# Optimization experiments

Measured on AMD Instinct MI355X. Metric: run time of the kernel, lower is better.

Reference implementation:

```python
import jax, jax.numpy as jnp
import numpy as np

B, DIM, OC, H, W, HEADS = 4, 128, 128, 128, 128, 8
L = H * W
_BN_INV = 1.0 / (1.0 + 1e-5) ** 0.5  # eval-mode BN: running_mean=0, running_var=1


def conv2d(x, w, b=None, groups=1, pad=0):
    y = jax.lax.conv_general_dilated(
        x, w, (1, 1), [(pad, pad), (pad, pad)],
        dimension_numbers=('NCHW', 'OIHW', 'NCHW'),
        feature_group_count=groups)
    if b is not None:
        y = y + b[None, :, None, None]
    return y


def bn(x, g, b):
    return x * (g * _BN_INV)[None, :, None, None] + b[None, :, None, None]


def ln(x, g, b, eps=1e-5):
    m = jnp.mean(x, -1, keepdims=True)
    v = jnp.mean((x - m) ** 2, -1, keepdims=True)
    return (x - m) * jax.lax.rsqrt(v + eps) * g + b


def rope_tables(h, w, c, base=10000.0):
    k_max = c // 4
    theta = 1.0 / base ** (np.arange(k_max, dtype=np.float32) / k_max)
    gi, gj = np.meshgrid(np.arange(h, dtype=np.float32),
                         np.arange(w, dtype=np.float32), indexing='ij')
    ang = np.concatenate([gi[..., None] * theta, gj[..., None] * theta], -1)  # (h,w,c//2)
    return jnp.asarray(np.cos(ang)), jnp.asarray(np.sin(ang))


def apply_rope(x, cs, sn):  # x: (b,h,w,c); consecutive pairs = (re, im)
    xr, xi = x[..., 0::2], x[..., 1::2]
    return jnp.stack([cs * xr - sn * xi, sn * xr + cs * xi], -1).reshape(x.shape)


def linear_attn(x, qk_w, qk_b, lepe_w, lepe_b, h, w):
    b, n, c = x.shape
    hd = c // HEADS
    qk = x @ qk_w.T + qk_b
    q = jax.nn.elu(qk[..., :c]) + 1.0
    k = jax.nn.elu(qk[..., c:]) + 1.0
    cs, sn = rope_tables(h, w, c)

    def heads(t):  # (b,n,c) -> (b,HEADS,n,hd)
        return t.reshape(b, n, HEADS, hd).transpose(0, 2, 1, 3)

    q_r = heads(apply_rope(q.reshape(b, h, w, c), cs, sn).reshape(b, n, c))
    k_r = heads(apply_rope(k.reshape(b, h, w, c), cs, sn).reshape(b, n, c))
    qh, kh, vh = heads(q), heads(k), heads(x)
    k_mean = jnp.mean(kh, axis=2, keepdims=True)                      # (b,Hd,1,hd)
    z = 1.0 / (jnp.einsum('bhnd,bhmd->bhnm', qh, k_mean) + 1e-6)      # (b,Hd,n,1)
    s = n ** -0.5
    kv = jnp.einsum('bhnd,bhne->bhde', k_r * s, vh * s)               # (b,Hd,hd,hd)
    out = jnp.einsum('bhnd,bhde->bhne', q_r, kv) * z
    out = out.transpose(0, 2, 1, 3).reshape(b, n, c)
    v_img = x.reshape(b, h, w, c).transpose(0, 3, 1, 2)
    lepe = conv2d(v_img, lepe_w, lepe_b, groups=c, pad=1)
    return out + lepe.transpose(0, 2, 3, 1).reshape(b, n, c)


def fmt_block(xb, fw1, fb1, f_g, f_be, fw2, fb2, n_g, n_be):
    t = jnp.fft.fft2(xb)                                              # (B,C,H,W) complex
    wgt = jax.nn.relu(bn(conv2d(t.real, fw1, fb1), f_g, f_be))
    wgt = jax.nn.sigmoid(conv2d(wgt, fw2, fb2))
    f = jnp.abs(jnp.fft.ifft2(wgt * t))
    f = jax.nn.relu(bn(f, n_g, n_be))
    return f.reshape(f.shape[0], f.shape[1], -1).transpose(0, 2, 1)   # (B,L,C)


def _forward(x, c1_w, c1_b, c1_g, c1_be, cpe1_w, cpe1_b,
             fw1, fb1, f_g, f_be, fw2, fb2, nbn_g, nbn_be,
             ln1_g, ln1_b, d3w1, d3b1, d3w2, d5w1, d5b1, d5w2,
             ap_w, ap_b, ip2_w, ip2_b, dwc2_w, dwc2_b,
             qk_w, qk_b, lepe_w, lepe_b, op_w, op_b,
             cpe2_w, cpe2_b, ln2_g, ln2_b,
             ffn_w1, ffn_b1, ffn_w2, ffn_b2, po_w,
             red_w, red_b, red_g, red_be):
    Bb, C, Hh, Ww = x.shape
    Ll = Hh * Ww
    to_img = lambda t: t.reshape(Bb, Hh, Ww, C).transpose(0, 3, 1, 2)   # (B,L,C)->(B,C,H,W)
    to_seq = lambda t: t.transpose(0, 2, 3, 1).reshape(Bb, Ll, -1)       # (B,C,H,W)->(B,L,C)

    x_0 = jax.nn.relu(bn(conv2d(x, c1_w, c1_b), c1_g, c1_be))           # (B,OC,H,W)
    xt = to_seq(x + conv2d(x, cpe1_w, cpe1_b, groups=C, pad=1))
    shortcut = xt
    fmt1 = fmt_block(to_img(xt), fw1, fb1, f_g, f_be, fw2, fb2, nbn_g, nbn_be)

    x_s = ln(xt, ln1_g, ln1_b)
    xs_img = to_img(x_s)
    x_s3 = conv2d(conv2d(xs_img, d3w1, d3b1), d3w2, None, groups=C // 2, pad=1)
    x_s5 = conv2d(conv2d(xs_img, d5w1, d5b1), d5w2, None, groups=C // 2, pad=2)
    act_res = jax.nn.silu(to_seq(conv2d(xs_img, ap_w, ap_b)))

    def branch(t):  # (B,C/2,H,W) -> (B,L,C/2)
        t = conv2d(t, ip2_w, ip2_b)
        t = jax.nn.silu(conv2d(t, dwc2_w, dwc2_b, groups=C // 2, pad=1))
        return to_seq(t)

    a3 = linear_attn(branch(x_s3), qk_w, qk_b, lepe_w, lepe_b, Hh, Ww)
    a5 = linear_attn(branch(x_s5), qk_w, qk_b, lepe_w, lepe_b, Hh, Ww)
    xs = jnp.concatenate([a3, a5], -1)
    xs = to_seq(conv2d(to_img(xs * act_res), op_w, op_b))

    xt = shortcut + xs + fmt1
    xt = xt + to_seq(conv2d(to_img(xt), cpe2_w, cpe2_b, groups=C, pad=1))
    fmt2 = fmt_block(to_img(xt), fw1, fb1, f_g, f_be, fw2, fb2, nbn_g, nbn_be)
    h2 = ln(xt, ln2_g, ln2_b)
    ffn = jax.nn.gelu(h2 @ ffn_w1.T + ffn_b1, approximate=False) @ ffn_w2.T + ffn_b2
    xt = xt + ffn + fmt2

    xo = conv2d(to_img(xt), po_w)                                        # (B,OC,H,W)
    cat = jnp.concatenate([x_0, xo], 1)
    return jax.nn.relu(bn(conv2d(cat, red_w, red_b), red_g, red_be)) + x_0


def setup_inputs():
    key = jax.random.key(0)
    it = iter(jax.random.split(key, 64))

    def w(shape, s=0.05):
        return jax.random.normal(next(it), shape, jnp.float32) * s

    d, oc = DIM, OC
    ones = lambda n: jnp.ones((n,), jnp.float32)
    zeros = lambda n: jnp.zeros((n,), jnp.float32)
    return {
        'x': jax.random.normal(next(it), (B, d, H, W), jnp.float32),
        'c1_w': w((oc, d, 1, 1)), 'c1_b': w((oc,), 0.01), 'c1_g': ones(oc), 'c1_be': zeros(oc),
        'cpe1_w': w((d, 1, 3, 3)), 'cpe1_b': w((d,), 0.01),
        'fw1': w((d // 16, d, 1, 1)), 'fb1': w((d // 16,), 0.01),
        'f_g': ones(d // 16), 'f_be': zeros(d // 16),
        'fw2': w((d, d // 16, 1, 1)), 'fb2': w((d,), 0.01),
        'nbn_g': ones(d), 'nbn_be': zeros(d),
        'ln1_g': ones(d), 'ln1_b': zeros(d),
        'd3w1': w((d, d, 1, 1)), 'd3b1': w((d,), 0.01), 'd3w2': w((d // 2, 2, 3, 3)),
        'd5w1': w((d, d, 1, 1)), 'd5b1': w((d,), 0.01), 'd5w2': w((d // 2, 2, 5, 5)),
        'ap_w': w((d, d, 1, 1)), 'ap_b': w((d,), 0.01),
        'ip2_w': w((d // 2, d // 2, 1, 1)), 'ip2_b': w((d // 2,), 0.01),
        'dwc2_w': w((d // 2, 1, 3, 3)), 'dwc2_b': w((d // 2,), 0.01),
        'qk_w': w((d, d // 2)), 'qk_b': w((d,), 0.01),
        'lepe_w': w((d // 2, 1, 3, 3)), 'lepe_b': w((d // 2,), 0.01),
        'op_w': w((d, d, 1, 1)), 'op_b': w((d,), 0.01),
        'cpe2_w': w((d, 1, 3, 3)), 'cpe2_b': w((d,), 0.01),
        'ln2_g': ones(d), 'ln2_b': zeros(d),
        'ffn_w1': w((4, d)), 'ffn_b1': w((4,), 0.01),
        'ffn_w2': w((d, 4)), 'ffn_b2': w((d,), 0.01),
        'po_w': w((oc, d, 1, 1)),
        'red_w': w((oc, 2 * oc, 1, 1)), 'red_b': w((oc,), 0.01),
        'red_g': ones(oc), 'red_be': zeros(oc),
    }


def reference(x, c1_w, c1_b, c1_g, c1_be, cpe1_w, cpe1_b,
              fw1, fb1, f_g, f_be, fw2, fb2, nbn_g, nbn_be,
              ln1_g, ln1_b, d3w1, d3b1, d3w2, d5w1, d5b1, d5w2,
              ap_w, ap_b, ip2_w, ip2_b, dwc2_w, dwc2_b,
              qk_w, qk_b, lepe_w, lepe_b, op_w, op_b,
              cpe2_w, cpe2_b, ln2_g, ln2_b,
              ffn_w1, ffn_b1, ffn_w2, ffn_b2, po_w,
              red_w, red_b, red_g, red_be):
    return _forward(x, c1_w, c1_b, c1_g, c1_be, cpe1_w, cpe1_b,
                    fw1, fb1, f_g, f_be, fw2, fb2, nbn_g, nbn_be,
                    ln1_g, ln1_b, d3w1, d3b1, d3w2, d5w1, d5b1, d5w2,
                    ap_w, ap_b, ip2_w, ip2_b, dwc2_w, dwc2_b,
                    qk_w, qk_b, lepe_w, lepe_b, op_w, op_b,
                    cpe2_w, cpe2_b, ln2_g, ln2_b,
                    ffn_w1, ffn_b1, ffn_w2, ffn_b2, po_w,
                    red_w, red_b, red_g, red_be)
```

## Files before the change

### kernel.cpp

```cpp
#include <hip/hip_runtime.h>
#include <math.h>

typedef unsigned short bf16_t;
typedef __attribute__((ext_vector_type(8))) short short8;
typedef __attribute__((ext_vector_type(4))) float f32x4;

#define B_ 4
#define C_ 128
#define H_ 128
#define W_ 128
#define L_ (H_*W_)
#define NS  ((size_t)B_*L_*C_)
#define NH  ((size_t)B_*L_*64)
#define NSP ((size_t)L_*C_)
#define PI_F 3.14159265358979323846f
#define BN_INV 0.9999950000374997f
#define THETA_SC 0.8304820237218406f
#define TOTW 157148
#define W16SHIFT 107548
#define WOFF_PO 107612
#define WOFF_RED 123996

#define W2_ 66
#define L2_ (128*W2_)
// ... 272 lines not shown
  __syncthreads();
  for (int i = tid; i < 4224; i += 256) {
    int h = i / 33, wl = i - h*33;
    rp[(size_t)h*W2_ + wl] = Lre[h][wl];
    ip[(size_t)h*W2_ + wl] = Lim[h][wl];
  }
}

__global__ __launch_bounds__(256) void k_fft_row_inv_abs_seq_h(
    const float* __restrict__ re, const float* __restrict__ im,
    const float* __restrict__ ng, const float* __restrict__ nbe,
    const float* __restrict__ add1, const float* __restrict__ add2,
    float* __restrict__ out) {
  __shared__ float S[64*132];
  int tid = threadIdx.x;
  int bid = blockIdx.x;
  int ch = (bid & 1) * 64;
  int h  = (bid >> 1) & 127;
  int b  = bid >> 8;
  {
    const float* rbase = re + (size_t)(b*128 + ch)*L2_ + (size_t)h*W2_;
    const float* ibase = im + (size_t)(b*128 + ch)*L2_ + (size_t)h*W2_;
    for (int i = tid; i < 64*66; i += 256) {
      int c = i / 66, v = i - c*66;
      S[c*132 + v]      = rbase[(size_t)c*L2_ + v];
      S[c*132 + 66 + v] = ibase[(size_t)c*L2_ + v];
    }
  }
  __syncthreads();
  int lane = tid & 63, wv = tid >> 6;
  int rb = (int)(__brev((unsigned)lane) >> 26);
  int vlo = 2*rb, vhi = vlo + 1;
  float tc[7], ts[7];
  tw_inv(lane, tc, ts);
  float rr[8][4];
  #pragma unroll
  for (int t = 0; t < 8; t++) {
    int ca = wv*16 + 2*t, cb = ca + 1;
    const float* Sa = S + ca*132;
    const float* Sb = S + cb*132;
    float lor, loi, hir, hii;
    if (vlo <= 64) {
      float ar = Sa[vlo], ai = Sa[66+vlo], br = Sb[vlo], bi = Sb[66+vlo];
      lor = ar - bi; loi = ai + br;
    } else {
      int u = 128 - vlo;
      float ar = Sa[u], ai = Sa[66+u], br = Sb[u], bi = Sb[66+u];
      lor = ar + bi; loi = br - ai;
    }
    if (vhi <= 64) {
      float ar = Sa[vhi], ai = Sa[66+vhi], br = Sb[vhi], bi = Sb[66+vhi];
      hir = ar - bi; hii = ai + br;
    } else {
      int u = 128 - vhi;
      float ar = Sa[u], ai = Sa[66+u], br = Sb[u], bi = Sb[66+u];
      hir = ar + bi; hii = br - ai;
    }
    fft128_inv(lor, loi, hir, hii, lane, tc, ts);
    rr[t][0] = fabsf(lor);
    rr[t][1] = fabsf(loi);
    rr[t][2] = fabsf(hir);
    rr[t][3] = fabsf(hii);
  }
  __syncthreads();
  float* T = S;
  #pragma unroll
  for (int t = 0; t < 8; t++) {
    int ca = wv*16 + 2*t, cb = ca + 1;
    float sga = ng[ch+ca]*BN_INV, sba = nbe[ch+ca];
    float sgb = ng[ch+cb]*BN_INV, sbb = nbe[ch+cb];
    T[ca*130 + lane]      = fmaxf(rr[t][0]*(1.f/128.f)*sga + sba, 0.f);
    T[cb*130 + lane]      = fmaxf(rr[t][1]*(1.f/128.f)*sgb + sbb, 0.f);
    T[ca*130 + 64 + lane] = fmaxf(rr[t][2]*(1.f/128.f)*sga + sba, 0.f);
    T[cb*130 + 64 + lane] = fmaxf(rr[t][3]*(1.f/128.f)*sgb + sbb, 0.f);
  }
  __syncthreads();
  size_t sb0 = ((size_t)b*L_ + (size_t)h*128)*128 + ch;
  #pragma unroll
  for (int it = 0; it < 8; it++) {
    int idx = it*256 + tid;
    int c4 = (idx & 15)*4, w = idx >> 4;
    size_t off = sb0 + (size_t)w*128 + c4;
    float4 v;
    v.x = T[(c4+0)*130 + w];
    v.y = T[(c4+1)*130 + w];
    v.z = T[(c4+2)*130 + w];
    v.w = T[(c4+3)*130 + w];
    float4 x1 = *(const float4*)(add1 + off);
    float4 x2 = *(const float4*)(add2 + off);
    v.x += x1.x + x2.x; v.y += x1.y + x2.y;
    v.z += x1.z + x2.z; v.w += x1.w + x2.w;
    *(float4*)(out + off) = v;
  }
}

__global__ __launch_bounds__(256) void k_freq1_h(const float* __restrict__ tre,
    const float* __restrict__ fw1, const float* __restrict__ fb1,
    const float* __restrict__ fg, const float* __restrict__ fbe,
    float* __restrict__ wg1) {
  __shared__ float w1s[1024];
  int tid = threadIdx.x;
  for (int i = tid; i < 1024; i += 256) w1s[i] = fw1[i];
  __syncthreads();
  size_t g = (size_t)blockIdx.x*256 + tid;
  int p = (int)(g % L2_);
  int b = (int)(g / L2_);
  const float* tp = tre + (size_t)b*128*L2_ + p;
  float acc[8];
  #pragma unroll
  for (int o = 0; o < 8; o++) acc[o] = 0.f;
  for (int c = 0; c < 128; c++) {
    float v = tp[(size_t)c*L2_];
    #pragma unroll
    for (int o = 0; o < 8; o++) acc[o] += w1s[o*128+c]*v;
  }
  size_t ob = (size_t)b*8*L2_ + p;
  #pragma unroll
  for (int o = 0; o < 8; o++) {
    float v = (acc[o] + fb1[o]) * (fg[o]*BN_INV) + fbe[o];
    wg1[ob + (size_t)o*L2_] = fmaxf(v, 0.f);
  }
}

template<bool DUAL>
__global__ void k_p2s(const void* __restrict__ src, float* __restrict__ dst,
                      const float* __restrict__ add1, const float* __restrict__ add2,
                      const int* __restrict__ flagp) {
  __shared__ float tile[32][33];
  int fl = DUAL ? *flagp : 1;
  int b = blockIdx.z;
  int p0 = blockIdx.x*32, c0 = blockIdx.y*32;
  int tx = threadIdx.x, ty = threadIdx.y;
  size_t base_in = (size_t)b*NSP;
  #pragma unroll
  for (int k = 0; k < 4; k++) {
    size_t off = base_in + (size_t)(c0+ty+8*k)*L_ + p0 + tx;
    float v;
    if (DUAL && !fl) v = ldf(((const bf16_t*)src)[off]);
    else             v = ((const float*)src)[off];
    tile[ty+8*k][tx] = v;
  }
  __syncthreads();
  size_t base = (size_t)b*NSP;
  #pragma unroll
  for (int k = 0; k < 4; k++) {
    size_t idx = base + (size_t)(p0+ty+8*k)*C_ + c0 + tx;
    float v = tile[tx][ty+8*k];
    if (add1) v += add1[idx];
    if (add2) v += add2[idx];
    dst[idx] = v;
  }
}

template<int CC, int MODE>
__global__ __launch_bounds__(256) void k_dw3(const float* __restrict__ in,
    const float* __restrict__ w, const float* __restrict__ bias,
    float* __restrict__ out) {
  __shared__ float wl[9*CC];
  int tid = threadIdx.x;
  for (int i = tid; i < 9*CC; i += 256) {
    int tap = i / CC, ch = i % CC;
    wl[i] = w[ch*9 + tap];
  }
  __syncthreads();
  size_t g = (size_t)blockIdx.x*256 + tid;
  int c = (int)(g & (CC-1));
  float wr[9];
  #pragma unroll
  for (int t = 0; t < 9; t++) wr[t] = wl[t*CC + c];
  size_t s = g / CC;
  int w0 = (int)(s & 31) * 4;
  int hp = (int)((s >> 5) & 127);
  int b  = (int)(s >> 12);
  const float* ip = in + (size_t)b*L_*CC + c;
  float bi = bias[c];
  float a0 = bi, a1 = bi, a2 = bi, a3 = bi;
  #pragma unroll
  for (int dh = -1; dh <= 1; dh++) {
    int h2 = hp + dh;
    if ((unsigned)h2 >= 128u) continue;
    const float* rp = ip + (size_t)h2*W_*CC;
    float px[6];
    #pragma unroll
    for (int x = 0; x < 6; x++) {
      int w2 = w0 - 1 + x;
      px[x] = ((unsigned)w2 < 128u) ? rp[(size_t)w2*CC] : 0.f;
    }
    #pragma unroll
    for (int dw = 0; dw < 3; dw++) {
      float f = wr[(dh+1)*3 + dw];
      a0 += f*px[dw];   a1 += f*px[dw+1];
      a2 += f*px[dw+2]; a3 += f*px[dw+3];
    }
  }
  size_t tb = (size_t)b*L_ + (size_t)hp*W_ + w0;
  if (MODE == 0) {
    out[(tb+0)*CC + c] = in[(tb+0)*CC + c] + a0;
    out[(tb+1)*CC + c] = in[(tb+1)*CC + c] + a1;
    out[(tb+2)*CC + c] = in[(tb+2)*CC + c] + a2;
    out[(tb+3)*CC + c] = in[(tb+3)*CC + c] + a3;
  } else {
    out[(tb+0)*CC + c] = a0 / (1.f + expf(-a0));
    out[(tb+1)*CC + c] = a1 / (1.f + expf(-a1));
    out[(tb+2)*CC + c] = a2 / (1.f + expf(-a2));
    out[(tb+3)*CC + c] = a3 / (1.f + expf(-a3));
  }
}

template<int K>
__global__ __launch_bounds__(256) void k_gconv(const bf16_t* __restrict__ in,
    const float* __restrict__ w, float* __restrict__ out) {
  __shared__ float wl[K*K*128];
  int tid = threadIdx.x;
  for (int i = tid; i < 128*K*K; i += 256) {
    int tap = i >> 7, ch = i & 127;
    wl[i] = w[ch*(K*K) + tap];
  }
  __syncthreads();
  size_t g = (size_t)blockIdx.x*256 + tid;
  int oc = (int)(g & 63);
  float wx[K*K], wy[K*K];
  #pragma unroll
  for (int t = 0; t < K*K; t++) {
    wx[t] = wl[t*128 + 2*oc];
    wy[t] = wl[t*128 + 2*oc + 1];
  }
  size_t s = g >> 6;
  int w0 = (int)(s & 31) * 4;
  int hp = (int)((s >> 5) & 127);
  int b  = (int)(s >> 12);
  const bf16_t* ip = in + (size_t)b*L_*128 + 2*oc;
  constexpr int P = K/2;
  float a0 = 0.f, a1 = 0.f, a2 = 0.f, a3 = 0.f;
  #pragma unroll
  for (int kh = 0; kh < K; kh++) {
    int h2 = hp + kh - P;
    if ((unsigned)h2 >= 128u) continue;
    const bf16_t* rp = ip + (size_t)h2*W_*128;
    float2 px[K+3];
    #pragma unroll
    for (int x = 0; x < K+3; x++) {
      int w2 = w0 - P + x;
      if ((unsigned)w2 < 128u) {
        unsigned uv = *(const unsigned*)(rp + (size_t)w2*128);
        px[x] = make_float2(ldf((bf16_t)(uv & 0xffffu)), ldf((bf16_t)(uv >> 16)));
      } else px[x] = make_float2(0.f, 0.f);
    }
    #pragma unroll
    for (int kw = 0; kw < K; kw++) {
      float fx = wx[kh*K + kw], fy = wy[kh*K + kw];
      a0 += fx*px[kw+0].x + fy*px[kw+0].y;
      a1 += fx*px[kw+1].x + fy*px[kw+1].y;
      a2 += fx*px[kw+2].x + fy*px[kw+2].y;
      a3 += fx*px[kw+3].x + fy*px[kw+3].y;
    }
  }
  size_t tb = (size_t)b*L_ + (size_t)hp*W_ + w0;
  out[(tb+0)*64 + oc] = a0;
  out[(tb+1)*64 + oc] = a1;
  out[(tb+2)*64 + oc] = a2;
  out[(tb+3)*64 + oc] = a3;
}

template<int CIN, int COUT, int EPI, bool MUL, bool OB16>
__global__ __launch_bounds__(256) void k_mfma_tok(
    const float* __restrict__ in, const bf16_t* __restrict__ mulp,
    const bf16_t* __restrict__ W16, const float* __restrict__ bias,
    void* __restrict__ out) {
  constexpr int NO = COUT/16;
  constexpr int KS = (CIN >= 128) ? 4 : (CIN/32);
  int tid = threadIdx.x;
  int lane = tid & 63, wv = tid >> 6;
  int m = lane & 15, q = lane >> 4;
  size_t t0 = (size_t)blockIdx.x*64 + (size_t)wv*16;
  f32x4 acc[NO];
  #pragma unroll
  for (int i = 0; i < NO; i++) acc[i] = (f32x4){0.f,0.f,0.f,0.f};
  for (int kc = 0; kc < CIN; kc += KS*32) {
    float4 A[KS][2];
    #pragma unroll
    for (int kk = 0; kk < KS; kk++) {
      const float* ap = in + (t0 + m)*CIN + kc + kk*32 + q*8;
      A[kk][0] = *(const float4*)ap;
      A[kk][1] = *(const float4*)(ap + 4);
    }
    if (MUL) {
      #pragma unroll
      for (int kk = 0; kk < KS; kk++) {
        const bf16_t* mp = mulp + (t0 + m)*CIN + kc + kk*32 + q*8;
        union { bf16_t u[8]; short8 v; } mv;
        mv.v = *(const short8*)mp;
        A[kk][0].x*=ldf(mv.u[0]); A[kk][0].y*=ldf(mv.u[1]);
        A[kk][0].z*=ldf(mv.u[2]); A[kk][0].w*=ldf(mv.u[3]);
        A[kk][1].x*=ldf(mv.u[4]); A[kk][1].y*=ldf(mv.u[5]);
        A[kk][1].z*=ldf(mv.u[6]); A[kk][1].w*=ldf(mv.u[7]);
      }
    }
    #pragma unroll
    for (int kk = 0; kk < KS; kk++) {
      union { short s[8]; short8 v; } af;
      af.s[0]=(short)f2b(A[kk][0].x); af.s[1]=(short)f2b(A[kk][0].y);
      af.s[2]=(short)f2b(A[kk][0].z); af.s[3]=(short)f2b(A[kk][0].w);
      af.s[4]=(short)f2b(A[kk][1].x); af.s[5]=(short)f2b(A[kk][1].y);
      af.s[6]=(short)f2b(A[kk][1].z); af.s[7]=(short)f2b(A[kk][1].w);
      #pragma unroll
      for (int o = 0; o < NO; o++) {
        short8 bf = *(const short8*)(W16 + (size_t)(o*16 + m)*CIN + kc + kk*32 + q*8);
        acc[o] = __builtin_amdgcn_mfma_f32_16x16x32_bf16(af.v, bf, acc[o], 0, 0, 0);
      }
    }
  }
  #pragma unroll
  for (int o = 0; o < NO; o++) {
    float bv = (EPI >= 1) ? bias[o*16 + m] : 0.f;
    #pragma unroll
    for (int r = 0; r < 4; r++) {
      int row = q*4 + r;
      float v = acc[o][r] + bv;
      if (EPI == 2) v = v / (1.f + expf(-v));
      if (EPI == 3) v = v > 0.f ? v + 1.f : expf(v);
      size_t idx = (t0 + row)*COUT + o*16 + m;
      if (OB16) ((bf16_t*)out)[idx] = f2b(v);
      else      ((float*)out)[idx] = v;
    }
  }
}

__global__ __launch_bounds__(256) void k_mfma_ln3(
    const float* __restrict__ in,
    const float* __restrict__ lng, const float* __restrict__ lnb,
    const bf16_t* __restrict__ Wd3, const float* __restrict__ bd3,
    const bf16_t* __restrict__ Wd5, const float* __restrict__ bd5,
    const bf16_t* __restrict__ Wap, const float* __restrict__ bap,
    bf16_t* __restrict__ outd3, bf16_t* __restrict__ outd5, bf16_t* __restrict__ outap) {
  __shared__ float gs[128], bs[128];
  __shared__ bf16_t T16[64*130];
  int tid = threadIdx.x;
  if (tid < 128) { gs[tid] = lng[tid]; bs[tid] = lnb[tid]; }
  __syncthreads();
  int lane = tid & 63, wv = tid >> 6;
  int m = lane & 15, q = lane >> 4;
  size_t t0 = (size_t)blockIdx.x*64 + (size_t)wv*16;
  size_t t0blk = (size_t)blockIdx.x*64;
  float4 A[4][2];
  #pragma unroll
  for (int kk = 0; kk < 4; kk++) {
    const float* ap = in + (t0 + m)*128 + kk*32 + q*8;
    A[kk][0] = *(const float4*)ap;
    A[kk][1] = *(const float4*)(ap + 4);
  }
  float s = 0.f, ss = 0.f;
  #pragma unroll
  for (int kk = 0; kk < 4; kk++)
    #pragma unroll
    for (int h = 0; h < 2; h++) {
      float4 v = A[kk][h];
      s  += v.x + v.y + v.z + v.w;
      ss += v.x*v.x + v.y*v.y + v.z*v.z + v.w*v.w;
    }
  s  += __shfl_xor(s, 16);  s  += __shfl_xor(s, 32);
  ss += __shfl_xor(ss, 16); ss += __shfl_xor(ss, 32);
  float mean = s*(1.f/128.f);
  float inv = rsqrtf(ss*(1.f/128.f) - mean*mean + 1e-5f);
  short8 af[4];
  #pragma unroll
  for (int kk = 0; kk < 4; kk++) {
    union { short sh[8]; short8 v; } u;
    #pragma unroll
    for (int h = 0; h < 2; h++) {
      const float* vp = (const float*)&A[kk][h];
      #pragma unroll
      for (int j = 0; j < 4; j++) {
        int c = kk*32 + q*8 + h*4 + j;
        float x = (vp[j] - mean)*inv*gs[c] + bs[c];
        u.sh[h*4+j] = (short)f2b(x);
      }
    }
    af[kk] = u.v;
  }
  f32x4 acc[24];
  #pragma unroll
  for (int i = 0; i < 24; i++) acc[i] = (f32x4){0.f,0.f,0.f,0.f};
  #pragma unroll
  for (int kk = 0; kk < 4; kk++) {
    #pragma unroll
    for (int o = 0; o < 8; o++) {
      size_t woff = (size_t)(o*16 + m)*128 + kk*32 + q*8;
      short8 b3 = *(const short8*)(Wd3 + woff);
      acc[o]    = __builtin_amdgcn_mfma_f32_16x16x32_bf16(af[kk], b3, acc[o],    0, 0, 0);
      short8 b5 = *(const short8*)(Wd5 + woff);
      acc[8+o]  = __builtin_amdgcn_mfma_f32_16x16x32_bf16(af[kk], b5, acc[8+o],  0, 0, 0);
      short8 ba = *(const short8*)(Wap + woff);
      acc[16+o] = __builtin_amdgcn_mfma_f32_16x16x32_bf16(af[kk], ba, acc[16+o], 0, 0, 0);
    }
  }
  #pragma unroll
  for (int mi = 0; mi < 3; mi++) {
    const float* bp = (mi == 0) ? bd3 : (mi == 1) ? bd5 : bap;
    bf16_t* op = (mi == 0) ? outd3 : (mi == 1) ? outd5 : outap;
    #pragma unroll
    for (int o = 0; o < 8; o++) {
      float bv = bp[o*16 + m];
      #pragma unroll
      for (int r = 0; r < 4; r++) {
        float v = acc[mi*8 + o][r] + bv;
        if (mi == 2) v = v / (1.f + expf(-v));
        T16[(wv*16 + q*4 + r)*130 + o*16 + m] = f2b(v);
      }
    }
    __syncthreads();
    for (int i = tid; i < 1024; i += 256) {
      int tok = i >> 4, c0 = (i & 15) * 8;
      union { bf16_t u[8]; short8 v; } pk;
      #pragma unroll
      for (int j = 0; j < 8; j++) pk.u[j] = T16[tok*130 + c0 + j];
      *(short8*)(op + (t0blk + tok)*128 + c0) = pk.v;
    }
    __syncthreads();
  }
}

__global__ __launch_bounds__(256) void k_mfma_c1(
    const float* __restrict__ in, const bf16_t* __restrict__ W16,
    const float* __restrict__ bias, const float* __restrict__ gam,
    const float* __restrict__ bet, float* __restrict__ out) {
  constexpr int NO = 8;
  int tid = threadIdx.x;
  int lane = tid & 63, wv = tid >> 6;
  int m = lane & 15, q = lane >> 4;
  size_t t0 = (size_t)blockIdx.x*64 + (size_t)wv*16;
  f32x4 acc[NO];
  #pragma unroll
  for (int i = 0; i < NO; i++) acc[i] = (f32x4){0.f,0.f,0.f,0.f};
  {
    float4 A[4][2];
    #pragma unroll
    for (int kk = 0; kk < 4; kk++) {
      const float* ap = in + (t0 + m)*128 + kk*32 + q*8;
      A[kk][0] = *(const float4*)ap;
      A[kk][1] = *(const float4*)(ap + 4);
    }
    #pragma unroll
    for (int kk = 0; kk < 4; kk++) {
      union { short s[8]; short8 v; } af;
      af.s[0]=(short)f2b(A[kk][0].x); af.s[1]=(short)f2b(A[kk][0].y);
      af.s[2]=(short)f2b(A[kk][0].z); af.s[3]=(short)f2b(A[kk][0].w);
      af.s[4]=(short)f2b(A[kk][1].x); af.s[5]=(short)f2b(A[kk][1].y);
      af.s[6]=(short)f2b(A[kk][1].z); af.s[7]=(short)f2b(A[kk][1].w);
      #pragma unroll
      for (int o = 0; o < NO; o++) {
        short8 bf = *(const short8*)(W16 + (size_t)(o*16 + m)*128 + kk*32 + q*8);
        acc[o] = __builtin_amdgcn_mfma_f32_16x16x32_bf16(af.v, bf, acc[o], 0, 0, 0);
      }
    }
  }
  #pragma unroll
  for (int o = 0; o < NO; o++) {
    int oc = o*16 + m;
    float bi = bias[oc], gm = gam[oc]*BN_INV, be = bet[oc];
    #pragma unroll
    for (int r = 0; r < 4; r++) {
      int row = q*4 + r;
      float v = acc[o][r] + bi;
      out[(t0 + row)*128 + oc] = fmaxf(v*gm + be, 0.f);
    }
  }
}

__global__ __launch_bounds__(256) void k_mfma_red(
    const float* __restrict__ x0s, const float* __restrict__ xt4,
    const bf16_t* __restrict__ W16, const float* __restrict__ bias,
    const float* __restrict__ gam, const float* __restrict__ bet,
    void* __restrict__ out, const int* __restrict__ flagp) {
  __shared__ float T[128*65];
  constexpr int NO = 8;
  int fl = *flagp;
  int tid = threadIdx.x;
  int lane = tid & 63, wv = tid >> 6;
  int m = lane & 15, q = lane >> 4;
  size_t t0 = (size_t)blockIdx.x*64;
  size_t tw = t0 + (size_t)wv*16;
  f32x4 acc[NO];
  #pragma unroll
  for (int i = 0; i < NO; i++) acc[i] = (f32x4){0.f,0.f,0.f,0.f};
  #pragma unroll
  for (int half = 0; half < 2; half++) {
    const float* src = half ? xt4 : x0s;
    float4 A[4][2];
    #pragma unroll
    for (int kk = 0; kk < 4; kk++) {
      const float* ap = src + (tw + m)*128 + kk*32 + q*8;
      A[kk][0] = *(const float4*)ap;
      A[kk][1] = *(const float4*)(ap + 4);
    }
    #pragma unroll
    for (int kk = 0; kk < 4; kk++) {
      union { short s[8]; short8 v; } af;
      af.s[0]=(short)f2b(A[kk][0].x); af.s[1]=(short)f2b(A[kk][0].y);
      af.s[2]=(short)f2b(A[kk][0].z); af.s[3]=(short)f2b(A[kk][0].w);
      af.s[4]=(short)f2b(A[kk][1].x); af.s[5]=(short)f2b(A[kk][1].y);
      af.s[6]=(short)f2b(A[kk][1].z); af.s[7]=(short)f2b(A[kk][1].w);
      #pragma unroll
      for (int o = 0; o < NO; o++) {
        short8 bf = *(const short8*)(W16 + (size_t)(o*16 + m)*256 + half*128 + kk*32 + q*8);
        acc[o] = __builtin_amdgcn_mfma_f32_16x16x32_bf16(af.v, bf, acc[o], 0, 0, 0);
      }
    }
  }
  #pragma unroll
  for (int ot = 0; ot < NO; ot++) {
    int o = ot*16 + m;
    float bi = bias[o], gm = gam[o]*BN_INV, be = bet[o];
    #pragma unroll
    for (int r = 0; r < 4; r++) {
      int row = q*4 + r;
      float v = acc[ot][r] + bi;
      v = fmaxf(v*gm + be, 0.f);
      v += x0s[(tw + row)*128 + o];
      T[o*65 + wv*16 + row] = v;
    }
  }
  __syncthreads();
  int b = (int)(t0 >> 14);
  int p0 = (int)(t0 & (L_-1));
  if (!fl) {
    bf16_t* op = (bf16_t*)out;
    for (int i = tid; i < 8192; i += 256) {
      int o = i >> 6, tk = i & 63;
      op[((size_t)b*128 + o)*L_ + p0 + tk] = f2b(T[o*65 + tk]);
    }
  } else {
    float* op = (float*)out;
    for (int i = tid; i < 8192; i += 256) {
      int o = i >> 6, tk = i & 63;
      op[((size_t)b*128 + o)*L_ + p0 + tk] = T[o*65 + tk];
    }
  }
}

__global__ __launch_bounds__(256) void k_ln_ffn(const float* __restrict__ in,
    const float* __restrict__ g, const float* __restrict__ be,
    const float* __restrict__ w1, const float* __restrict__ b1,
    const float* __restrict__ w2, const float* __restrict__ b2,
    float* __restrict__ out) {
  int tid = threadIdx.x, lane = tid & 63;
  size_t t = (size_t)blockIdx.x*4 + (tid >> 6);
  const float* row = in + t*128;
  float2 v = *(const float2*)(row + lane*2);
  float s = v.x + v.y, ss = v.x*v.x + v.y*v.y;
  #pragma unroll
  for (int m = 1; m < 64; m <<= 1) { s += __shfl_xor(s, m); ss += __shfl_xor(ss, m); }
  float mean = s*(1.f/128.f);
  float inv = rsqrtf(ss*(1.f/128.f) - mean*mean + 1e-5f);
  float hx = (v.x-mean)*inv*g[lane*2]   + be[lane*2];
  float hy = (v.y-mean)*inv*g[lane*2+1] + be[lane*2+1];
  float hp0 = hx*w1[0*128+lane*2] + hy*w1[0*128+lane*2+1];
  float hp1 = hx*w1[1*128+lane*2] + hy*w1[1*128+lane*2+1];
  float hp2 = hx*w1[2*128+lane*2] + hy*w1[2*128+lane*2+1];
  float hp3 = hx*w1[3*128+lane*2] + hy*w1[3*128+lane*2+1];
  #pragma unroll
  for (int m = 1; m < 64; m <<= 1) {
    hp0 += __shfl_xor(hp0, m); hp1 += __shfl_xor(hp1, m);
    hp2 += __shfl_xor(hp2, m); hp3 += __shfl_xor(hp3, m);
  }
  float hv0, hv1, hv2, hv3;
  { float a = hp0 + b1[0]; hv0 = 0.5f*a*(1.f+erff(a*0.7071067811865476f)); }
  { float a = hp1 + b1[1]; hv1 = 0.5f*a*(1.f+erff(a*0.7071067811865476f)); }
  { float a = hp2 + b1[2]; hv2 = 0.5f*a*(1.f+erff(a*0.7071067811865476f)); }
  { float a = hp3 + b1[3]; hv3 = 0.5f*a*(1.f+erff(a*0.7071067811865476f)); }
  int cx = lane*2, cy = lane*2+1;
  float2 o;
  o.x = hv0*w2[cx*4+0] + hv1*w2[cx*4+1] + hv2*w2[cx*4+2] + hv3*w2[cx*4+3] + b2[cx];
  o.y = hv0*w2[cy*4+0] + hv1*w2[cy*4+1] + hv2*w2[cy*4+2] + hv3*w2[cy*4+3] + b2[cy];
  *(float2*)(out + t*128 + lane*2) = o;
}

__global__ __launch_bounds__(256) void k_kv(
    const bf16_t* __restrict__ qk, const float* __restrict__ v,
    float* __restrict__ akv_g, float* __restrict__ aks_g) {
  __shared__ float kvred[512];
  __shared__ float ksred[64];
  int tid = threadIdx.x;
  for (int i = tid; i < 512; i += 256) kvred[i] = 0.f;
  if (tid < 64) ksred[tid] = 0.f;
  __syncthreads();
  int lane = tid & 63, wv = tid >> 6;
  size_t t0 = (size_t)blockIdx.x * 64;
  int b = (int)(t0 >> 14);
  int pr = lane >> 1;
  float theta = exp2f(-(float)(pr & 15) * THETA_SC);
  bool use_i = pr < 16;
  int hbase = lane & 56;
  float akv[8];
  #pragma unroll
  for (int d = 0; d < 8; d++) akv[d] = 0.f;
  float aks = 0.f;
  for (int it = 0; it < 16; it++) {
    size_t t = t0 + (size_t)wv*16 + it;
    float k = ldf(qk[t*128 + 64 + lane]);
    float xv = v[t*64 + lane];
    int l = (int)(t & (L_-1));
    float pos = use_i ? (float)(l >> 7) : (float)(l & 127);
    float sn, cs; sincosf(pos*theta, &sn, &cs);
    float kp = __shfl_xor(k, 1);
    float kr = (lane & 1) ? (sn*kp + cs*k) : (cs*k - sn*kp);
    #pragma unroll
    for (int d = 0; d < 8; d++) {
      float krd = __shfl(kr, hbase + d);
      akv[d] += krd * xv;
    }
    aks += k;
  }
  int h8 = lane >> 3, e = lane & 7;
  #pragma unroll
  for (int d = 0; d < 8; d++)
    atomicAdd(&kvred[h8*64 + d*8 + e], akv[d]);
  atomicAdd(&ksred[lane], aks);
  __syncthreads();
  for (int i = tid; i < 512; i += 256) atomicAdd(&akv_g[b*512 + i], kvred[i]);
  if (tid < 64) atomicAdd(&aks_g[b*64 + tid], ksred[tid]);
}

__global__ __launch_bounds__(256) void k_attn2(
    const bf16_t* __restrict__ qk, const float* __restrict__ x,
    const float* __restrict__ akv_g, const float* __restrict__ aks_g,
    const float* __restrict__ lw, const float* __restrict__ lb,
    float* __restrict__ out, int coff) {
  __shared__ float kv[512];
  __shared__ float km[64];
  __shared__ float lwl[576];
  int tid = threadIdx.x;
  size_t t0 = (size_t)blockIdx.x * 32;
  int b = (int)(t0 >> 14);
  const float invn = 1.f/16384.f;
  for (int i = tid; i < 512; i += 256) kv[i] = akv_g[b*512 + i]*invn;
  if (tid < 64) km[tid] = aks_g[b*64 + tid]*invn;
  for (int i = tid; i < 576; i += 256) lwl[i] = lw[i];
  __syncthreads();
  int lane = tid & 63, wv = tid >> 6;
  int pr = lane >> 1;
  float theta = exp2f(-(float)(pr & 15) * THETA_SC);
  bool use_i = pr < 16;
  int hbase = lane & 56, e = lane & 7;
  float lbv = lb[lane];
  const float* xb = x + ((size_t)b << 14) * 64;
  for (int it = 0; it < 8; it++) {
    size_t t = t0 + (size_t)wv*8 + it;
    int l = (int)(t & (L_-1));
    int ipos = l >> 7, jpos = l & 127;
    float q = ldf(qk[t*128 + lane]);
    float p = q * km[lane];
    p += __shfl_xor(p, 1); p += __shfl_xor(p, 2); p += __shfl_xor(p, 4);
    float z = 1.f/(p + 1e-6f);
    float pos = use_i ? (float)ipos : (float)jpos;
    float sn, cs; sincosf(pos*theta, &sn, &cs);
    float qp = __shfl_xor(q, 1);
    float qr = (lane & 1) ? (sn*qp + cs*q) : (cs*q - sn*qp);
    float acc = 0.f;
    #pragma unroll
    for (int d = 0; d < 8; d++) {
      float qrd = __shfl(qr, hbase + d);
      acc += qrd * kv[hbase*8 + d*8 + e];
    }
    acc *= z;
    float lp = lbv;
    #pragma unroll
    for (int dh = -1; dh <= 1; dh++) {
      int h2 = ipos + dh; if ((unsigned)h2 >= 128u) continue;
      #pragma unroll
      for (int dw = -1; dw <= 1; dw++) {
        int w2 = jpos + dw; if ((unsigned)w2 >= 128u) continue;
        lp += lwl[lane*9 + (dh+1)*3 + (dw+1)] * xb[((size_t)(h2 << 7) + w2)*64 + lane];
      }
    }
    out[t*128 + coff + lane] = acc + lp;
  }
}

extern "C" void kernel_launch(void* const* d_in, const int* in_sizes, int n_in,
                              void* d_out, int out_size, void* d_ws, size_t ws_size,
                              hipStream_t stream) {
  (void)in_sizes; (void)n_in; (void)out_size;

  float* base;
  if (ws_size >= WSF * sizeof(float)) {
    base = (float*)d_ws;
  } else {
    void* p = nullptr;
    hipGetSymbolAddress(&p, HIP_SYMBOL(g_ws));
    base = (float*)p;
  }
  float* P0 = base;
  float* PA = base + 1*NS;
  float* PB = base + 2*NS;
  float* PC = base + 3*NS;
  float* PD = base + 4*NS;
  float* PF = base + 5*NS;
  float* H0 = base + 6*NS;
  float* H1 = H0 + NH;
  float* H2 = H1 + NH;
  float* WG = H2 + NH;
  float* ACC = WG + WGSLOT;
  float* CW  = ACC + ACCSZ;
  bf16_t* CW16 = (bf16_t*)(CW + CWSZ);
  int*   FLG = (int*)(CW + CWSZ + CW16SZF);

  static const int wsz[47] = {
    16384,128,128,128,1152,128,1024,8,8,8,1024,128,128,128,128,128,
    16384,128,1152,16384,128,3200,16384,128,4096,64,576,64,8192,128,
    576,64,16384,128,1152,128,128,128,512,4,512,128,16384,32768,128,128,128};
  int woff[47]; { int a = 0; for (int i = 0; i < 47; i++){ woff[i] = a; a += wsz[i]; } }
  const float* Wf[47]; for (int i = 0; i < 47; i++) Wf[i] = CW + woff[i];
  auto W16 = [&](int i){ return (const bf16_t*)(CW16 + woff[i] + (woff[i] >= W16SHIFT ? 4 : 0)); };
  const float *c1_b=Wf[1], *c1_g=Wf[2], *c1_be=Wf[3], *cpe1_w=Wf[4],
    *cpe1_b=Wf[5], *fw1=Wf[6], *fb1=Wf[7], *f_g=Wf[8], *f_be=Wf[9], *fw2=Wf[10],
    *fb2=Wf[11], *nbn_g=Wf[12], *nbn_be=Wf[13], *ln1_g=Wf[14], *ln1_b=Wf[15],
    *d3b1=Wf[17], *d3w2=Wf[18], *d5b1=Wf[20],
    *d5w2=Wf[21], *ap_b=Wf[23], *ip2_b=Wf[25],
    *dwc2_w=Wf[26], *dwc2_b=Wf[27], *qk_b=Wf[29], *lepe_w=Wf[30],
    *lepe_b=Wf[31], *op_b=Wf[33], *cpe2_w=Wf[34], *cpe2_b=Wf[35],
    *ln2_g=Wf[36], *ln2_b=Wf[37], *ffn_w1=Wf[38], *ffn_b1=Wf[39], *ffn_w2=Wf[40],
    *ffn_b2=Wf[41], *red_b=Wf[44], *red_g=Wf[45], *red_be=Wf[46];
  const bf16_t *c1_w16=W16(0), *d3w1_16=W16(16), *d5w1_16=W16(19), *ap_w16=W16(22),
    *ip2_w16=W16(24), *qk_w16=W16(28), *op_w16=W16(32), *red_w16=W16(43);

  const void* x = d_in[0];

  k_probe<<<1, 256, 0, stream>>>((const bf16_t*)x, FLG);
  P47 ps; for (int i = 0; i < 47; i++) ps.p[i] = d_in[i+1];
  k_cvt<<<(TOTW+255)/256, 256, 0, stream>>>(ps, FLG, CW);
  k_cvt16<<<(TOTW+255)/256, 256, 0, stream>>>(CW, CW16);
  k_fuse_red<<<64, 256, 0, stream>>>(CW + WOFF_PO, CW + WOFF_RED,
                                     (bf16_t*)(CW16 + WOFF_RED + 4));

  dim3 tgrid(512, 4, 4), tblk(32, 8);

  auto fmt_fused = [&](const float* seq_in, float* re, float* im,
                       const float* add1, const float* add2, float* outp) {
    k_fft_row_fwd_half<<<1024, 256, 0, stream>>>(seq_in, re, im);
    k_fft_col_fwd_h<<<1024, 256, 0, stream>>>(re, im);
    k_freq1_h<<<132, 256, 0, stream>>>(re, fw1, fb1, f_g, f_be, WG);
    k_fft_col_inv_scaled_h<<<1024, 256, 0, stream>>>(re, im, WG, fw2, fb2);
    k_fft_row_inv_abs_seq_h<<<1024, 256, 0, stream>>>(re, im, nbn_g, nbn_be, add1, add2, outp);
  };

  auto attn = [&](const float* brin, float* qkbuf, int coff) {
    k_zero<<<9, 256, 0, stream>>>(ACC, 2304);
    k_mfma_tok<64,128,3,false,true><<<1024, 256, 0, stream>>>(brin, nullptr, qk_w16, qk_b, qkbuf);
    k_kv<<<1024, 256, 0, stream>>>((const bf16_t*)qkbuf, brin, ACC, ACC + B_*512);
    k_attn2<<<2048, 256, 0, stream>>>((const bf16_t*)qkbuf, brin, ACC, ACC + B_*512, lepe_w, lepe_b, PF, coff);
  };

  k_p2s<true><<<tgrid, tblk, 0, stream>>>(x, PA, nullptr, nullptr, FLG);
  k_mfma_c1<<<1024, 256, 0, stream>>>(PA, c1_w16, c1_b, c1_g, c1_be, P0);
  k_dw3<128,0><<<8192, 256, 0, stream>>>(PA, cpe1_w, cpe1_b, PB);
  k_mfma_ln3<<<1024, 256, 0, stream>>>(PB, ln1_g, ln1_b,
      d3w1_16, d3b1, d5w1_16, d5b1, ap_w16, ap_b,
      (bf16_t*)PD, (bf16_t*)PF, (bf16_t*)PA);
  k_gconv<3><<<4096, 256, 0, stream>>>((const bf16_t*)PD, d3w2, H0);
  k_gconv<5><<<4096, 256, 0, stream>>>((const bf16_t*)PF, d5w2, H1);
  k_mfma_tok<64,64,1,false,false><<<1024, 256, 0, stream>>>(H0, nullptr, ip2_w16, ip2_b, H2);
  k_dw3<64,1><<<4096, 256, 0, stream>>>(H2, dwc2_w, dwc2_b, H0);
  attn(H0, PD, 0);
  k_mfma_tok<64,64,1,false,false><<<1024, 256, 0, stream>>>(H1, nullptr, ip2_w16, ip2_b, H2);
  k_dw3<64,1><<<4096, 256, 0, stream>>>(H2, dwc2_w, dwc2_b, H1);
  attn(H1, PD, 64);
  k_mfma_tok<128,128,1,true,false><<<1024, 256, 0, stream>>>(PF, (const bf16_t*)PA, op_w16, op_b, PF);
  fmt_fused(PB, PC, PD, PB, PF, PB);
  k_dw3<128,0><<<8192, 256, 0, stream>>>(PB, cpe2_w, cpe2_b, PC);
  k_ln_ffn<<<16384, 256, 0, stream>>>(PC, ln2_g, ln2_b, ffn_w1, ffn_b1, ffn_w2, ffn_b2, PF);
  fmt_fused(PC, PB, PD, PC, PF, PC);
  k_mfma_red<<<1024, 256, 0, stream>>>(P0, PC, red_w16, red_b, red_g, red_be, d_out, FLG);
}
```

Baseline: 922.1 us.

## Store intermediate branch activations and conv1 output in bf16

```diff
diff --git a/kernel.cpp b/kernel.cpp
--- a/kernel.cpp
+++ b/kernel.cpp
@@ -448,7 +448,7 @@
   }
 }
 
-template<int CC, int MODE>
+template<int CC>
 __global__ __launch_bounds__(256) void k_dw3(const float* __restrict__ in,
     const float* __restrict__ w, const float* __restrict__ bias,
     float* __restrict__ out) {
@@ -490,22 +490,62 @@
     }
   }
   size_t tb = (size_t)b*L_ + (size_t)hp*W_ + w0;
-  if (MODE == 0) {
-    out[(tb+0)*CC + c] = in[(tb+0)*CC + c] + a0;
-    out[(tb+1)*CC + c] = in[(tb+1)*CC + c] + a1;
-    out[(tb+2)*CC + c] = in[(tb+2)*CC + c] + a2;
-    out[(tb+3)*CC + c] = in[(tb+3)*CC + c] + a3;
-  } else {
-    out[(tb+0)*CC + c] = a0 / (1.f + expf(-a0));
-    out[(tb+1)*CC + c] = a1 / (1.f + expf(-a1));
-    out[(tb+2)*CC + c] = a2 / (1.f + expf(-a2));
-    out[(tb+3)*CC + c] = a3 / (1.f + expf(-a3));
-  }
+  out[(tb+0)*CC + c] = in[(tb+0)*CC + c] + a0;
+  out[(tb+1)*CC + c] = in[(tb+1)*CC + c] + a1;
+  out[(tb+2)*CC + c] = in[(tb+2)*CC + c] + a2;
+  out[(tb+3)*CC + c] = in[(tb+3)*CC + c] + a3;
+}
+
+__global__ __launch_bounds__(256) void k_dw3h(const bf16_t* __restrict__ in,
+    const float* __restrict__ w, const float* __restrict__ bias,
+    bf16_t* __restrict__ out) {
+  __shared__ float wl[9*64];
+  int tid = threadIdx.x;
+  for (int i = tid; i < 9*64; i += 256) {
+    int tap = i / 64, ch = i % 64;
+    wl[i] = w[ch*9 + tap];
+  }
+  __syncthreads();
+  size_t g = (size_t)blockIdx.x*256 + tid;
+  int c = (int)(g & 63);
+  float wr[9];
+  #pragma unroll
+  for (int t = 0; t < 9; t++) wr[t] = wl[t*64 + c];
+  size_t s = g >> 6;
+  int w0 = (int)(s & 31) * 4;
+  int hp = (int)((s >> 5) & 127);
+  int b  = (int)(s >> 12);
+  const bf16_t* ip = in + (size_t)b*L_*64 + c;
+  float bi = bias[c];
+  float a0 = bi, a1 = bi, a2 = bi, a3 = bi;
+  #pragma unroll
+  for (int dh = -1; dh <= 1; dh++) {
+    int h2 = hp + dh;
+    if ((unsigned)h2 >= 128u) continue;
+    const bf16_t* rp = ip + (size_t)h2*W_*64;
+    float px[6];
+    #pragma unroll
+    for (int x = 0; x < 6; x++) {
+      int w2 = w0 - 1 + x;
+      px[x] = ((unsigned)w2 < 128u) ? ldf(rp[(size_t)w2*64]) : 0.f;
+    }
+    #pragma unroll
+    for (int dw = 0; dw < 3; dw++) {
+      float f = wr[(dh+1)*3 + dw];
+      a0 += f*px[dw];   a1 += f*px[dw+1];
+      a2 += f*px[dw+2]; a3 += f*px[dw+3];
+    }
+  }
+  size_t tb = (size_t)b*L_ + (size_t)hp*W_ + w0;
+  out[(tb+0)*64 + c] = f2b(a0 / (1.f + expf(-a0)));
+  out[(tb+1)*64 + c] = f2b(a1 / (1.f + expf(-a1)));
+  out[(tb+2)*64 + c] = f2b(a2 / (1.f + expf(-a2)));
+  out[(tb+3)*64 + c] = f2b(a3 / (1.f + expf(-a3)));
 }
 
 template<int K>
 __global__ __launch_bounds__(256) void k_gconv(const bf16_t* __restrict__ in,
-    const float* __restrict__ w, float* __restrict__ out) {
+    const float* __restrict__ w, bf16_t* __restrict__ out) {
   __shared__ float wl[K*K*128];
   int tid = threadIdx.x;
   for (int i = tid; i < 128*K*K; i += 256) {
@@ -552,15 +592,15 @@
     }
   }
   size_t tb = (size_t)b*L_ + (size_t)hp*W_ + w0;
-  out[(tb+0)*64 + oc] = a0;
-  out[(tb+1)*64 + oc] = a1;
-  out[(tb+2)*64 + oc] = a2;
-  out[(tb+3)*64 + oc] = a3;
-}
-
-template<int CIN, int COUT, int EPI, bool MUL, bool OB16>
+  out[(tb+0)*64 + oc] = f2b(a0);
+  out[(tb+1)*64 + oc] = f2b(a1);
+  out[(tb+2)*64 + oc] = f2b(a2);
+  out[(tb+3)*64 + oc] = f2b(a3);
+}
+
+template<int CIN, int COUT, int EPI, bool MUL, bool IB16, bool OB16>
 __global__ __launch_bounds__(256) void k_mfma_tok(
-    const float* __restrict__ in, const bf16_t* __restrict__ mulp,
+    const void* __restrict__ in, const bf16_t* __restrict__ mulp,
     const bf16_t* __restrict__ W16, const float* __restrict__ bias,
     void* __restrict__ out) {
   constexpr int NO = COUT/16;
@@ -573,36 +613,47 @@
   #pragma unroll
   for (int i = 0; i < NO; i++) acc[i] = (f32x4){0.f,0.f,0.f,0.f};
   for (int kc = 0; kc < CIN; kc += KS*32) {
-    float4 A[KS][2];
-    #pragma unroll
-    for (int kk = 0; kk < KS; kk++) {
-      const float* ap = in + (t0 + m)*CIN + kc + kk*32 + q*8;
-      A[kk][0] = *(const float4*)ap;
-      A[kk][1] = *(const float4*)(ap + 4);
-    }
-    if (MUL) {
+    short8 afv[KS];
+    if (IB16) {
+      #pragma unroll
+      for (int kk = 0; kk < KS; kk++)
+        afv[kk] = *(const short8*)((const bf16_t*)in + (t0 + m)*CIN + kc + kk*32 + q*8);
+    } else {
+      float4 A[KS][2];
       #pragma unroll
       for (int kk = 0; kk < KS; kk++) {
-        const bf16_t* mp = mulp + (t0 + m)*CIN + kc + kk*32 + q*8;
-        union { bf16_t u[8]; short8 v; } mv;
-        mv.v = *(const short8*)mp;
-        A[kk][0].x*=ldf(mv.u[0]); A[kk][0].y*=ldf(mv.u[1]);
-        A[kk][0].z*=ldf(mv.u[2]); A[kk][0].w*=ldf(mv.u[3]);
-        A[kk][1].x*=ldf(mv.u[4]); A[kk][1].y*=ldf(mv.u[5]);
-        A[kk][1].z*=ldf(mv.u[6]); A[kk][1].w*=ldf(mv.u[7]);
+        const float* ap = (const float*)in + (t0 + m)*CIN + kc + kk*32 + q*8;
+        A[kk][0] = *(const float4*)ap;
+        A[kk][1] = *(const float4*)(ap + 4);
       }
+      if (MUL) {
+        #pragma unroll
+        for (int kk = 0; kk < KS; kk++) {
+          const bf16_t* mp = mulp + (t0 + m)*CIN + kc + kk*32 + q*8;
+          union { bf16_t u[8]; short8 v; } mv;
+          mv.v = *(const short8*)mp;
+          A[kk][0].x*=ldf(mv.u[0]); A[kk][0].y*=ldf(mv.u[1]);
+          A[kk][0].z*=ldf(mv.u[2]); A[kk][0].w*=ldf(mv.u[3]);
+          A[kk][1].x*=ldf(mv.u[4]); A[kk][1].y*=ldf(mv.u[5]);
+          A[kk][1].z*=ldf(mv.u[6]); A[kk][1].w*=ldf(mv.u[7]);
+        }
+      }
+      #pragma unroll
+      for (int kk = 0; kk < KS; kk++) {
+        union { short s[8]; short8 v; } af;
+        af.s[0]=(short)f2b(A[kk][0].x); af.s[1]=(short)f2b(A[kk][0].y);
+        af.s[2]=(short)f2b(A[kk][0].z); af.s[3]=(short)f2b(A[kk][0].w);
+        af.s[4]=(short)f2b(A[kk][1].x); af.s[5]=(short)f2b(A[kk][1].y);
+        af.s[6]=(short)f2b(A[kk][1].z); af.s[7]=(short)f2b(A[kk][1].w);
+        afv[kk] = af.v;
+      }
     }
     #pragma unroll
     for (int kk = 0; kk < KS; kk++) {
-      union { short s[8]; short8 v; } af;
-      af.s[0]=(short)f2b(A[kk][0].x); af.s[1]=(short)f2b(A[kk][0].y);
-      af.s[2]=(short)f2b(A[kk][0].z); af.s[3]=(short)f2b(A[kk][0].w);
-      af.s[4]=(short)f2b(A[kk][1].x); af.s[5]=(short)f2b(A[kk][1].y);
-      af.s[6]=(short)f2b(A[kk][1].z); af.s[7]=(short)f2b(A[kk][1].w);
       #pragma unroll
       for (int o = 0; o < NO; o++) {
         short8 bf = *(const short8*)(W16 + (size_t)(o*16 + m)*CIN + kc + kk*32 + q*8);
-        acc[o] = __builtin_amdgcn_mfma_f32_16x16x32_bf16(af.v, bf, acc[o], 0, 0, 0);
+        acc[o] = __builtin_amdgcn_mfma_f32_16x16x32_bf16(afv[kk], bf, acc[o], 0, 0, 0);
       }
     }
   }
@@ -719,12 +770,14 @@
 __global__ __launch_bounds__(256) void k_mfma_c1(
     const float* __restrict__ in, const bf16_t* __restrict__ W16,
     const float* __restrict__ bias, const float* __restrict__ gam,
-    const float* __restrict__ bet, float* __restrict__ out) {
+    const float* __restrict__ bet, bf16_t* __restrict__ out) {
+  __shared__ bf16_t T16[64*130];
   constexpr int NO = 8;
   int tid = threadIdx.x;
   int lane = tid & 63, wv = tid >> 6;
   int m = lane & 15, q = lane >> 4;
   size_t t0 = (size_t)blockIdx.x*64 + (size_t)wv*16;
+  size_t t0blk = (size_t)blockIdx.x*64;
   f32x4 acc[NO];
   #pragma unroll
   for (int i = 0; i < NO; i++) acc[i] = (f32x4){0.f,0.f,0.f,0.f};
@@ -756,15 +809,22 @@
     float bi = bias[oc], gm = gam[oc]*BN_INV, be = bet[oc];
     #pragma unroll
     for (int r = 0; r < 4; r++) {
-      int row = q*4 + r;
       float v = acc[o][r] + bi;
-      out[(t0 + row)*128 + oc] = fmaxf(v*gm + be, 0.f);
-    }
+      T16[(wv*16 + q*4 + r)*130 + oc] = f2b(fmaxf(v*gm + be, 0.f));
+    }
+  }
+  __syncthreads();
+  for (int i = tid; i < 1024; i += 256) {
+    int tok = i >> 4, c0 = (i & 15) * 8;
+    union { bf16_t u[8]; short8 v; } pk;
+    #pragma unroll
+    for (int j = 0; j < 8; j++) pk.u[j] = T16[tok*130 + c0 + j];
+    *(short8*)(out + (t0blk + tok)*128 + c0) = pk.v;
   }
 }
 
 __global__ __launch_bounds__(256) void k_mfma_red(
-    const float* __restrict__ x0s, const float* __restrict__ xt4,
+    const bf16_t* __restrict__ x0s, const float* __restrict__ xt4,
     const bf16_t* __restrict__ W16, const float* __restrict__ bias,
     const float* __restrict__ gam, const float* __restrict__ bet,
     void* __restrict__ out, const int* __restrict__ flagp) {
@@ -780,12 +840,19 @@
   #pragma unroll
   for (int i = 0; i < NO; i++) acc[i] = (f32x4){0.f,0.f,0.f,0.f};
   #pragma unroll
-  for (int half = 0; half < 2; half++) {
-    const float* src = half ? xt4 : x0s;
+  for (int kk = 0; kk < 4; kk++) {
+    short8 afv = *(const short8*)(x0s + (tw + m)*128 + kk*32 + q*8);
+    #pragma unroll
+    for (int o = 0; o < NO; o++) {
+      short8 bf = *(const short8*)(W16 + (size_t)(o*16 + m)*256 + kk*32 + q*8);
+      acc[o] = __builtin_amdgcn_mfma_f32_16x16x32_bf16(afv, bf, acc[o], 0, 0, 0);
+    }
+  }
+  {
     float4 A[4][2];
     #pragma unroll
     for (int kk = 0; kk < 4; kk++) {
-      const float* ap = src + (tw + m)*128 + kk*32 + q*8;
+      const float* ap = xt4 + (tw + m)*128 + kk*32 + q*8;
       A[kk][0] = *(const float4*)ap;
       A[kk][1] = *(const float4*)(ap + 4);
     }
@@ -798,7 +865,7 @@
       af.s[6]=(short)f2b(A[kk][1].z); af.s[7]=(short)f2b(A[kk][1].w);
       #pragma unroll
       for (int o = 0; o < NO; o++) {
-        short8 bf = *(const short8*)(W16 + (size_t)(o*16 + m)*256 + half*128 + kk*32 + q*8);
+        short8 bf = *(const short8*)(W16 + (size_t)(o*16 + m)*256 + 128 + kk*32 + q*8);
         acc[o] = __builtin_amdgcn_mfma_f32_16x16x32_bf16(af.v, bf, acc[o], 0, 0, 0);
       }
     }
@@ -812,7 +879,7 @@
       int row = q*4 + r;
       float v = acc[ot][r] + bi;
       v = fmaxf(v*gm + be, 0.f);
-      v += x0s[(tw + row)*128 + o];
+      v += ldf(x0s[(tw + row)*128 + o]);
       T[o*65 + wv*16 + row] = v;
     }
   }
@@ -872,7 +939,7 @@
 }
 
 __global__ __launch_bounds__(256) void k_kv(
-    const bf16_t* __restrict__ qk, const float* __restrict__ v,
+    const bf16_t* __restrict__ qk, const bf16_t* __restrict__ v,
     float* __restrict__ akv_g, float* __restrict__ aks_g) {
   __shared__ float kvred[512];
   __shared__ float ksred[64];
@@ -894,7 +961,7 @@
   for (int it = 0; it < 16; it++) {
     size_t t = t0 + (size_t)wv*16 + it;
     float k = ldf(qk[t*128 + 64 + lane]);
-    float xv = v[t*64 + lane];
+    float xv = ldf(v[t*64 + lane]);
     int l = (int)(t & (L_-1));
     float pos = use_i ? (float)(l >> 7) : (float)(l & 127);
     float sn, cs; sincosf(pos*theta, &sn, &cs);
@@ -918,7 +985,7 @@
 }
 
 __global__ __launch_bounds__(256) void k_attn2(
-    const bf16_t* __restrict__ qk, const float* __restrict__ x,
+    const bf16_t* __restrict__ qk, const bf16_t* __restrict__ x,
     const float* __restrict__ akv_g, const float* __restrict__ aks_g,
     const float* __restrict__ lw, const float* __restrict__ lb,
     float* __restrict__ out, int coff) {
@@ -939,7 +1006,7 @@
   bool use_i = pr < 16;
   int hbase = lane & 56, e = lane & 7;
   float lbv = lb[lane];
-  const float* xb = x + ((size_t)b << 14) * 64;
+  const bf16_t* xb = x + ((size_t)b << 14) * 64;
   for (int it = 0; it < 8; it++) {
     size_t t = t0 + (size_t)wv*8 + it;
     int l = (int)(t & (L_-1));
@@ -966,7 +1033,7 @@
       #pragma unroll
       for (int dw = -1; dw <= 1; dw++) {
         int w2 = jpos + dw; if ((unsigned)w2 >= 128u) continue;
-        lp += lwl[lane*9 + (dh+1)*3 + (dw+1)] * xb[((size_t)(h2 << 7) + w2)*64 + lane];
+        lp += lwl[lane*9 + (dh+1)*3 + (dw+1)] * ldf(xb[((size_t)(h2 << 7) + w2)*64 + lane]);
       }
     }
     out[t*128 + coff + lane] = acc + lp;
@@ -1040,31 +1107,31 @@
     k_fft_row_inv_abs_seq_h<<<1024, 256, 0, stream>>>(re, im, nbn_g, nbn_be, add1, add2, outp);
   };
 
-  auto attn = [&](const float* brin, float* qkbuf, int coff) {
+  auto attn = [&](const bf16_t* brin, float* qkbuf, int coff) {
     k_zero<<<9, 256, 0, stream>>>(ACC, 2304);
-    k_mfma_tok<64,128,3,false,true><<<1024, 256, 0, stream>>>(brin, nullptr, qk_w16, qk_b, qkbuf);
+    k_mfma_tok<64,128,3,false,true,true><<<1024, 256, 0, stream>>>(brin, nullptr, qk_w16, qk_b, qkbuf);
     k_kv<<<1024, 256, 0, stream>>>((const bf16_t*)qkbuf, brin, ACC, ACC + B_*512);
     k_attn2<<<2048, 256, 0, stream>>>((const bf16_t*)qkbuf, brin, ACC, ACC + B_*512, lepe_w, lepe_b, PF, coff);
   };
 
   k_p2s<true><<<tgrid, tblk, 0, stream>>>(x, PA, nullptr, nullptr, FLG);
-  k_mfma_c1<<<1024, 256, 0, stream>>>(PA, c1_w16, c1_b, c1_g, c1_be, P0);
-  k_dw3<128,0><<<8192, 256, 0, stream>>>(PA, cpe1_w, cpe1_b, PB);
+  k_mfma_c1<<<1024, 256, 0, stream>>>(PA, c1_w16, c1_b, c1_g, c1_be, (bf16_t*)P0);
+  k_dw3<128><<<8192, 256, 0, stream>>>(PA, cpe1_w, cpe1_b, PB);
   k_mfma_ln3<<<1024, 256, 0, stream>>>(PB, ln1_g, ln1_b,
       d3w1_16, d3b1, d5w1_16, d5b1, ap_w16, ap_b,
       (bf16_t*)PD, (bf16_t*)PF, (bf16_t*)PA);
-  k_gconv<3><<<4096, 256, 0, stream>>>((const bf16_t*)PD, d3w2, H0);
-  k_gconv<5><<<4096, 256, 0, stream>>>((const bf16_t*)PF, d5w2, H1);
-  k_mfma_tok<64,64,1,false,false><<<1024, 256, 0, stream>>>(H0, nullptr, ip2_w16, ip2_b, H2);
-  k_dw3<64,1><<<4096, 256, 0, stream>>>(H2, dwc2_w, dwc2_b, H0);
-  attn(H0, PD, 0);
-  k_mfma_tok<64,64,1,false,false><<<1024, 256, 0, stream>>>(H1, nullptr, ip2_w16, ip2_b, H2);
-  k_dw3<64,1><<<4096, 256, 0, stream>>>(H2, dwc2_w, dwc2_b, H1);
-  attn(H1, PD, 64);
-  k_mfma_tok<128,128,1,true,false><<<1024, 256, 0, stream>>>(PF, (const bf16_t*)PA, op_w16, op_b, PF);
+  k_gconv<3><<<4096, 256, 0, stream>>>((const bf16_t*)PD, d3w2, (bf16_t*)H0);
+  k_gconv<5><<<4096, 256, 0, stream>>>((const bf16_t*)PF, d5w2, (bf16_t*)H1);
+  k_mfma_tok<64,64,1,false,true,true><<<1024, 256, 0, stream>>>((const bf16_t*)H0, nullptr, ip2_w16, ip2_b, (bf16_t*)H2);
+  k_dw3h<<<4096, 256, 0, stream>>>((const bf16_t*)H2, dwc2_w, dwc2_b, (bf16_t*)H0);
+  attn((const bf16_t*)H0, PD, 0);
+  k_mfma_tok<64,64,1,false,true,true><<<1024, 256, 0, stream>>>((const bf16_t*)H1, nullptr, ip2_w16, ip2_b, (bf16_t*)H2);
+  k_dw3h<<<4096, 256, 0, stream>>>((const bf16_t*)H2, dwc2_w, dwc2_b, (bf16_t*)H1);
+  attn((const bf16_t*)H1, PD, 64);
+  k_mfma_tok<128,128,1,true,false,false><<<1024, 256, 0, stream>>>(PF, (const bf16_t*)PA, op_w16, op_b, PF);
   fmt_fused(PB, PC, PD, PB, PF, PB);
-  k_dw3<128,0><<<8192, 256, 0, stream>>>(PB, cpe2_w, cpe2_b, PC);
+  k_dw3<128><<<8192, 256, 0, stream>>>(PB, cpe2_w, cpe2_b, PC);
   k_ln_ffn<<<16384, 256, 0, stream>>>(PC, ln2_g, ln2_b, ffn_w1, ffn_b1, ffn_w2, ffn_b2, PF);
   fmt_fused(PC, PB, PD, PC, PF, PC);
-  k_mfma_red<<<1024, 256, 0, stream>>>(P0, PC, red_w16, red_b, red_g, red_be, d_out, FLG);
-}
+  k_mfma_red<<<1024, 256, 0, stream>>>((const bf16_t*)P0, PC, red_w16, red_b, red_g, red_be, d_out, FLG);
+}
```

Result: no change. 914.0 us (-0.9%).
